# Performance work log

Hardware: AMD Instinct MI355X
Metric: run time of the kernel (lower is better)

## Reference

```python
import jax, jax.numpy as jnp
import numpy as np

EPS = 1e-6

def _rms_norm(x, w):
    # torch: x / (||x||_2 * n^{-1/2} + eps) * w
    rms = jnp.linalg.norm(x, axis=-1, keepdims=True) * (x.shape[-1] ** -0.5)
    return x / (rms + EPS) * w

def _rope_cos_sin(seq_len, head_dim):
    half = head_dim // 2
    freq = 1.0 / (10000.0 ** (jnp.arange(half, dtype=jnp.float32) / half))
    t = jnp.arange(seq_len, dtype=jnp.float32)
    freqs = t[:, None] * freq[None, :]            # [s, half]
    freqs = jnp.concatenate([freqs, freqs], -1)   # [s, d_head]
    cos = jnp.cos(freqs)[None, :, None, :]        # [1, s, 1, d_head]
    sin = jnp.sin(freqs)[None, :, None, :]
    return cos, sin

def _rotate_half(x):
    h = x.shape[-1] // 2
    return jnp.concatenate([-x[..., h:], x[..., :h]], -1)

def setup_inputs() -> dict:
    key = jax.random.key(0)
    ks = jax.random.split(key, 8)
    B, S, D, H, F = 2, 2048, 2048, 16, 128
    return {
        'query_input': jax.random.normal(ks[0], (B, S, D), jnp.float32),
        'key_input':   jax.random.normal(ks[1], (B, S, D), jnp.float32),
        'value_input': jax.random.normal(ks[2], (B, S, D), jnp.float32),
        'W_Q': jax.random.normal(ks[3], (H, D, F), jnp.float32) * (D ** -0.5),
        'W_K': jax.random.normal(ks[4], (H, D, F), jnp.float32) * (D ** -0.5),
        'W_V': jax.random.normal(ks[5], (H, D, F), jnp.float32) * (D ** -0.5),
        'W_O': jax.random.normal(ks[6], (H, F, D), jnp.float32) * (F ** -0.5),
        'b_Q': jnp.zeros((H, F), jnp.float32),
        'b_K': jnp.zeros((H, F), jnp.float32),
        'b_V': jnp.zeros((H, F), jnp.float32),
        'b_O': jnp.zeros((D,), jnp.float32),
        'q_norm_w': jnp.ones((F,), jnp.float32),
        'k_norm_w': jnp.ones((F,), jnp.float32),
    }

def reference(query_input, key_input, value_input, W_Q, W_K, W_V, W_O,
              b_Q, b_K, b_V, b_O, q_norm_w, k_norm_w):
    head_dim = W_Q.shape[-1]
    q = jnp.einsum('bpd,hdf->bphf', query_input, W_Q) + b_Q[None, None]
    k = jnp.einsum('bpd,hdf->bphf', key_input,   W_K) + b_K[None, None]
    v = jnp.einsum('bpd,hdf->bphf', value_input, W_V) + b_V[None, None]
    q = _rms_norm(q, q_norm_w)
    k = _rms_norm(k, k_norm_w)
    cos, sin = _rope_cos_sin(q.shape[1], head_dim)
    q = q * cos + _rotate_half(q) * sin
    k = k * cos + _rotate_half(k) * sin
    scores = jnp.einsum('bphf,bqhf->bhpq', q, k) / (head_dim ** 0.5)
    pattern = jax.nn.softmax(scores, axis=-1)
    attn = jnp.einsum('bhpq,bqhf->bphf', pattern, v)
    return jnp.einsum('bphf,hfm->bpm', attn, W_O) + b_O
```

## Files before the change

kernel.cpp:

```cpp
#include <hip/hip_runtime.h>
#include <stdint.h>

typedef unsigned short u16;
typedef __attribute__((ext_vector_type(8))) short  s8b;
typedef __attribute__((ext_vector_type(4))) float  f32x4;

#define S_LEN   2048
#define NHEAD   16
#define HD      128
#define DM      2048
#define NB      2
#define NPLANE  (NB*NHEAD)
#define ROWS    (NB*S_LEN)
#define PLANE_ELEMS (S_LEN*HD)
#define ATT_SCALE 0.08838834764831845f
#define LOG2E     1.4426950408889634f

__device__ __forceinline__ float bf2f(u16 u){
  union { unsigned u; float f; } x; x.u = ((unsigned)u) << 16; return x.f;
}
__device__ __forceinline__ u16 f2bf(float f){
  union { float f; unsigned u; } x; x.f = f;
  unsigned r = x.u + 0x7FFFu + ((x.u >> 16) & 1u);
  return (u16)(r >> 16);
}
__device__ __forceinline__ unsigned cvtpk(float lo, float hi){
  unsigned r;
  asm("v_cvt_pk_bf16_f32 %0, %1, %2" : "=v"(r) : "v"(lo), "v"(hi));
  return r;
}

typedef const __attribute__((address_space(1))) unsigned int* gas1;
typedef __attribute__((address_space(3))) unsigned int* las3;
__device__ __forceinline__ void gload16(const void* g, void* l){
  __builtin_amdgcn_global_load_lds((gas1)g, (las3)l, 16, 0, 0);
}

__device__ __forceinline__ f32x4 mfma16(s8b a, s8b b, f32x4 c){
  return __builtin_amdgcn_mfma_f32_16x16x32_bf16(a, b, c, 0, 0, 0);
}

__global__ __launch_bounds__(256) void cvt4(const float4* __restrict__ in,
                                            uint2* __restrict__ out, int n4){
  int i = blockIdx.x*256 + threadIdx.x;
  if (i >= n4) return;
  float4 v = in[i];
  uint2 o;
  o.x = (unsigned)f2bf(v.x) | ((unsigned)f2bf(v.y) << 16);
  o.y = (unsigned)f2bf(v.z) | ((unsigned)f2bf(v.w) << 16);
  out[i] = o;
}

__global__ __launch_bounds__(256) void transpose_cvt(const float* __restrict__ in,
                                                     u16* __restrict__ out,
                                                     int R, int C, int outStride){
  __shared__ float tile[32][33];
  int z = blockIdx.z;
  const float* inz = in + (size_t)z * R * C;
  u16* outz = out + (size_t)z * C * outStride;
  int r0 = blockIdx.x*32, c0 = blockIdx.y*32;
  int tx = threadIdx.x, ty = threadIdx.y;
  #pragma unroll
  for (int i=0;i<4;i++)
    tile[ty*4+i][tx] = inz[(size_t)(r0+ty*4+i)*C + c0 + tx];
  __syncthreads();
  #pragma unroll
  for (int i=0;i<4;i++)
    outz[(size_t)(c0+ty*4+i)*outStride + r0 + tx] = f2bf(tile[tx][ty*4+i]);
}

__global__ __launch_bounds__(256) void rope_tab(float* __restrict__ ctab,
                                                float* __restrict__ stab){
  int i = blockIdx.x*256 + threadIdx.x;
  int p = i >> 6, j = i & 63;
  double freq = pow(10000.0, -(double)j / 64.0);
  double a = (double)p * freq;
  ctab[i] = (float)cos(a);
  stab[i] = (float)sin(a);
}

__global__ __launch_bounds__(256) void gemm_bt(const u16* __restrict__ A,
                                               const u16* __restrict__ BT,
                                               const float* __restrict__ bias,
                                               void* __restrict__ out, int mode){
  const int K = 2048;
  __shared__ u16 As[2][4096];
  __shared__ u16 Bs[2][4096];
  const int t = threadIdx.x, w = t >> 6, l = t & 63;
  const int lr = l & 15, lg = l >> 4;
  int bid = blockIdx.x;
  int swz = (bid & 7)*64 + (bid >> 3);
  const int M0 = (swz >> 4) * 128, N0 = (swz & 15) * 128;
  const int wr = w >> 1, wc = w & 1;

  f32x4 acc[4][4];
  #pragma unroll
  for (int i=0;i<4;i++)
    #pragma unroll
    for (int j=0;j<4;j++) acc[i][j] = f32x4{0.f,0.f,0.f,0.f};

  auto stage = [&](int buf, int kt){
    #pragma unroll
    for (int c=0;c<2;c++){
      int mloc = c*64 + w*16 + (l>>2);
      int kloc = (l&3)*8;
      gload16(A  + (size_t)(M0+mloc)*K + kt*32 + kloc, &As[buf][c*2048 + w*512]);
      gload16(BT + (size_t)(N0+mloc)*K + kt*32 + kloc, &Bs[buf][c*2048 + w*512]);
    }
  };

  stage(0, 0);
  int cur = 0;
  const int NT = K/32;
  for (int kt=0; kt<NT; kt++){
    __syncthreads();
    if (kt+1 < NT) stage(cur^1, kt+1);
    s8b af[4], bf[4];
    #pragma unroll
    for (int i=0;i<4;i++){
      af[i] = *(const s8b*)&As[cur][(wr*64 + i*16 + lr)*32 + lg*8];
      bf[i] = *(const s8b*)&Bs[cur][(wc*64 + i*16 + lr)*32 + lg*8];
    }
    __builtin_amdgcn_s_setprio(1);
    #pragma unroll
    for (int i=0;i<4;i++)
      #pragma unroll
      for (int j=0;j<4;j++)
        acc[i][j] = mfma16(af[i], bf[j], acc[i][j]);
    __builtin_amdgcn_s_setprio(0);
    cur ^= 1;
  }

  #pragma unroll
  for (int i=0;i<4;i++){
    int growb = M0 + wr*64 + i*16 + lg*4;
    #pragma unroll
    for (int j=0;j<4;j++){
      int gcol = N0 + wc*64 + j*16 + lr;
      float bv = bias[gcol];
      #pragma unroll
      for (int r=0;r<4;r++){
        int grow = growb + r;
        float v = acc[i][j][r] + bv;
        if (mode == 2){
          ((float*)out)[(size_t)grow*2048 + gcol] = v;
        } else {
          int b = grow >> 11, p = grow & 2047;
          int h = gcol >> 7,  f = gcol & 127;
          if (mode == 0){
            ((u16*)out)[(((size_t)(b*NHEAD+h))*S_LEN + p)*HD + f] = f2bf(v);
          } else {
            size_t base = ((size_t)(b*NHEAD+h)*PLANE_ELEMS + (size_t)(p>>6)*8192) * 2;
            int p6 = p & 63;
            int q_ = ((p6&12)<<1) | (p6&3) | ((p6&16)>>2);
            int kvp = (p6 & 32) | q_;
            int byte = (f*128 + kvp*2) ^ ((f&7)<<4);
            *(u16*)((char*)out + base + byte) = f2bf(v);
          }
        }
      }
    }
  }
}

__global__ __launch_bounds__(256) void norm_rope(const u16* __restrict__ in,
                                                 u16* __restrict__ outp,
                                                 const float* __restrict__ nw,
                                                 const float* __restrict__ ctab,
                                                 const float* __restrict__ stab,
                                                 int swizzled, float oscale){
  int t = threadIdx.x, w = t>>6, l = t&63;
  size_t R = (size_t)blockIdx.x*4 + w;
  int p = (int)(R & (S_LEN-1));
  size_t base = R * HD;
  float x0 = bf2f(in[base + l]);
  float x1 = bf2f(in[base + 64 + l]);
  float ss = x0*x0 + x1*x1;
  #pragma unroll
  for (int m=1;m<64;m<<=1) ss += __shfl_xor(ss, m);
  float rms = sqrtf(ss * (1.0f/128.0f));
  float sc = oscale / (rms + 1e-6f);
  float xn0 = x0 * sc * nw[l];
  float xn1 = x1 * sc * nw[64+l];
  float c = ctab[(size_t)p*64 + l], s = stab[(size_t)p*64 + l];
  float o0 = xn0*c - xn1*s;
  float o1 = xn1*c + xn0*s;
  if (!swizzled){
    outp[base + l]      = f2bf(o0);
    outp[base + 64 + l] = f2bf(o1);
  } else {
    size_t plane = R >> 11;
    int kv = p & 63;
    size_t tb = (plane*(size_t)PLANE_ELEMS + (size_t)(p>>6)*8192) * 2;
    int b0 = (kv*256 + l*2)        ^ ((kv&7)<<4);
    int b1 = (kv*256 + (64+l)*2)   ^ ((kv&7)<<4);
    *(u16*)((char*)outp + tb + b0) = f2bf(o0);
    *(u16*)((char*)outp + tb + b1) = f2bf(o1);
  }
}

__global__ __launch_bounds__(512) void attn_fwd(const u16* __restrict__ qn,
                                                const u16* __restrict__ kn,
                                                const u16* __restrict__ vt,
                                                u16* __restrict__ attn_out){
  __shared__ u16 Klds[2][8192];
  __shared__ u16 Vlds[2][8192];
  int t = threadIdx.x, w = t>>6, l = t&63;
  int lr = l&15, lg = l>>4;

  int bid = blockIdx.x;
  int xcd = bid & 7, j = bid >> 3;
  int plane = xcd*4 + (j >> 4);
  int qb = j & 15;
  int q0 = qb*128 + w*16;

  s8b qf[4];
  #pragma unroll
  for (int fc=0; fc<4; fc++)
    qf[fc] = *(const s8b*)(qn + ((size_t)plane*S_LEN + q0 + lr)*HD + fc*32 + lg*8);

  float m = -1e30f, lsum = 0.f;
  f32x4 oacc[8];
  #pragma unroll
  for (int i=0;i<8;i++) oacc[i] = f32x4{0.f,0.f,0.f,0.f};

  const u16* kbase = kn + (size_t)plane*PLANE_ELEMS;
  const u16* vbase = vt + (size_t)plane*PLANE_ELEMS;

  auto stage = [&](int buf, int kt){
    #pragma unroll
    for (int i=0;i<2;i++){
      gload16(kbase + (size_t)kt*8192 + w*1024 + i*512 + l*8, &Klds[buf][w*1024 + i*512]);
      gload16(vbase + (size_t)kt*8192 + w*1024 + i*512 + l*8, &Vlds[buf][w*1024 + i*512]);
    }
  };

  stage(0, 0);
  int cur = 0;
  for (int kt=0; kt<32; kt++){
    __syncthreads();
    if (kt+1 < 32) stage(cur^1, kt+1);

    f32x4 sacc[4];
    #pragma unroll
    for (int c=0;c<4;c++) sacc[c] = f32x4{0.f,0.f,0.f,0.f};
    __builtin_amdgcn_s_setprio(1);
    #pragma unroll
    for (int c=0;c<4;c++){
      int kv = c*16 + lr;
      #pragma unroll
      for (int fc=0; fc<4; fc++){
        int byte = (kv*256 + (fc*32 + lg*8)*2) ^ ((kv&7)<<4);
        s8b kf = *(const s8b*)((const char*)&Klds[cur][0] + byte);
        sacc[c] = mfma16(kf, qf[fc], sacc[c]);
      }
    }
    __builtin_amdgcn_s_setprio(0);

    float mx01 = fmaxf(fmaxf(sacc[0][0], sacc[0][1]), fmaxf(sacc[0][2], sacc[0][3]));
    float mx11 = fmaxf(fmaxf(sacc[1][0], sacc[1][1]), fmaxf(sacc[1][2], sacc[1][3]));
    float mx21 = fmaxf(fmaxf(sacc[2][0], sacc[2][1]), fmaxf(sacc[2][2], sacc[2][3]));
    float mx31 = fmaxf(fmaxf(sacc[3][0], sacc[3][1]), fmaxf(sacc[3][2], sacc[3][3]));
    float mx = fmaxf(fmaxf(mx01, mx11), fmaxf(mx21, mx31));
    if (__any(mx > m + 11.5f)){
      float v = mx;
      v = fmaxf(v, __shfl_xor(v, 16));
      v = fmaxf(v, __shfl_xor(v, 32));
      v = fmaxf(m, v);
      float al = exp2f(m - v);
      m = v; lsum *= al;
      float alr[4];
      #pragma unroll
      for (int r=0;r<4;r++) alr[r] = __shfl(al, lg*4 + r);
      #pragma unroll
      for (int i=0;i<8;i++)
        #pragma unroll
        for (int r=0;r<4;r++) oacc[i][r] *= alr[r];
    }
    float pv[4][4];
    float ls0 = 0.f, ls1 = 0.f, ls2 = 0.f, ls3 = 0.f;
    #pragma unroll
    for (int c=0;c<4;c++){
      float e0 = exp2f(sacc[c][0] - m);
      float e1 = exp2f(sacc[c][1] - m);
      float e2 = exp2f(sacc[c][2] - m);
      float e3 = exp2f(sacc[c][3] - m);
      pv[c][0]=e0; pv[c][1]=e1; pv[c][2]=e2; pv[c][3]=e3;
      ls0 += e0; ls1 += e1; ls2 += e2; ls3 += e3;
    }
    lsum += (ls0 + ls1) + (ls2 + ls3);

    s8b pa[2];
    #pragma unroll
    for (int kc=0;kc<2;kc++){
      union { s8b v; unsigned u[4]; } pu;
      pu.u[0] = cvtpk(pv[2*kc][0],   pv[2*kc][1]);
      pu.u[1] = cvtpk(pv[2*kc][2],   pv[2*kc][3]);
      pu.u[2] = cvtpk(pv[2*kc+1][0], pv[2*kc+1][1]);
      pu.u[3] = cvtpk(pv[2*kc+1][2], pv[2*kc+1][3]);
      pa[kc] = pu.v;
    }

    __builtin_amdgcn_s_setprio(1);
    #pragma unroll
    for (int kc=0;kc<2;kc++){
      #pragma unroll
      for (int fc2=0; fc2<8; fc2++){
        int f = fc2*16 + lr;
        int byte = (f*128 + (kc*32 + lg*8)*2) ^ ((f&7)<<4);
        s8b vf = *(const s8b*)((const char*)&Vlds[cur][0] + byte);
        oacc[fc2] = mfma16(pa[kc], vf, oacc[fc2]);
      }
    }
    __builtin_amdgcn_s_setprio(0);
    cur ^= 1;
  }

  {
    float v = lsum;
    v += __shfl_xor(v, 16);
    v += __shfl_xor(v, 32);
    lsum = 1.0f / v;
  }
  float lir[4];
  #pragma unroll
  for (int r=0;r<4;r++) lir[r] = __shfl(lsum, lg*4 + r);
  int b = plane >> 4, h = plane & 15;
  #pragma unroll
  for (int fc2=0; fc2<8; fc2++){
    int f = fc2*16 + lr;
    #pragma unroll
    for (int r=0;r<4;r++){
      int row = q0 + lg*4 + r;
      float v = oacc[fc2][r] * lir[r];
      attn_out[(((size_t)b*S_LEN + row)*NHEAD + h)*HD + f] = f2bf(v);
    }
  }
}

extern "C" void kernel_launch(void* const* d_in, const int* in_sizes, int n_in,
                              void* d_out, int out_size, void* d_ws, size_t ws_size,
                              hipStream_t stream){
  const float* xq = (const float*)d_in[0];
  const float* xk = (const float*)d_in[1];
  const float* xv = (const float*)d_in[2];
  const float* WQ = (const float*)d_in[3];
  const float* WK = (const float*)d_in[4];
  const float* WV = (const float*)d_in[5];
  const float* WO = (const float*)d_in[6];
  const float* bQ = (const float*)d_in[7];
  const float* bK = (const float*)d_in[8];
  const float* bV = (const float*)d_in[9];
  const float* bO = (const float*)d_in[10];
  const float* qw = (const float*)d_in[11];
  const float* kw = (const float*)d_in[12];

  char* ws = (char*)d_ws;
  size_t off = 0;
  auto alloc = [&](size_t bytes)->void*{
    void* p = ws + off; off += (bytes + 255) & ~(size_t)255; return p;
  };
  const size_t ACT = (size_t)ROWS*DM*2;
  const size_t WMT = (size_t)DM*DM*2;
  u16* xqb  = (u16*)alloc(ACT);
  u16* xkb  = (u16*)alloc(ACT);
  u16* xvb  = (u16*)alloc(ACT);
  u16* WqT  = (u16*)alloc(WMT);
  u16* WkT  = (u16*)alloc(WMT);
  u16* WvT  = (u16*)alloc(WMT);
  u16* WoT  = (u16*)alloc(WMT);
  u16* qraw = (u16*)alloc(ACT);
  u16* kraw = (u16*)alloc(ACT);
  u16* knT  = (u16*)alloc(ACT);
  u16* vtS  = (u16*)alloc(ACT);
  u16* attn = (u16*)alloc(ACT);
  float* ctab = (float*)alloc((size_t)S_LEN*64*4);
  float* stab = (float*)alloc((size_t)S_LEN*64*4);
  if (off > ws_size) return;

  const int n4 = ROWS*DM/4;
  cvt4<<<dim3(n4/256), dim3(256), 0, stream>>>((const float4*)xq, (uint2*)xqb, n4);
  cvt4<<<dim3(n4/256), dim3(256), 0, stream>>>((const float4*)xk, (uint2*)xkb, n4);
  cvt4<<<dim3(n4/256), dim3(256), 0, stream>>>((const float4*)xv, (uint2*)xvb, n4);
  rope_tab<<<dim3(S_LEN*64/256), dim3(256), 0, stream>>>(ctab, stab);
  transpose_cvt<<<dim3(64,4,16), dim3(32,8), 0, stream>>>(WQ, WqT, 2048, 128, 2048);
  transpose_cvt<<<dim3(64,4,16), dim3(32,8), 0, stream>>>(WK, WkT, 2048, 128, 2048);
  transpose_cvt<<<dim3(64,4,16), dim3(32,8), 0, stream>>>(WV, WvT, 2048, 128, 2048);
  transpose_cvt<<<dim3(64,64,1), dim3(32,8), 0, stream>>>(WO, WoT, 2048, 2048, 2048);

  gemm_bt<<<dim3(512), dim3(256), 0, stream>>>(xqb, WqT, bQ, qraw, 0);
  gemm_bt<<<dim3(512), dim3(256), 0, stream>>>(xkb, WkT, bK, kraw, 0);
  gemm_bt<<<dim3(512), dim3(256), 0, stream>>>(xvb, WvT, bV, vtS, 1);

  norm_rope<<<dim3(NPLANE*S_LEN/4), dim3(256), 0, stream>>>(qraw, qraw, qw, ctab, stab, 0, ATT_SCALE*LOG2E);
  norm_rope<<<dim3(NPLANE*S_LEN/4), dim3(256), 0, stream>>>(kraw, knT, kw, ctab, stab, 1, 1.0f);

  attn_fwd<<<dim3(512), dim3(512), 0, stream>>>(qraw, knT, vtS, attn);

  gemm_bt<<<dim3(512), dim3(256), 0, stream>>>(attn, WoT, bO, d_out, 2);
}
```

Measured before the change: 397.2 us.

## Merge input conversions, use float rope table, unroll GEMM and attention loops by two

Folds the three fp32-to-bf16 input conversion launches into a single launch that picks its tensor from blockIdx.y, cutting launch overhead. The rope table now uses single-precision exp2f/cosf/sinf in place of double-precision pow/cos/sin, which is cheaper but slightly less accurate at large angles. The GEMM and attention main loops are unrolled by two with fixed double-buffer indices, removing the runtime buffer toggle and the per-iteration bound check on the first stage call.

```diff
diff --git a/kernel.cpp b/kernel.cpp
--- a/kernel.cpp
+++ b/kernel.cpp
@@ -40,15 +40,21 @@
   return __builtin_amdgcn_mfma_f32_16x16x32_bf16(a, b, c, 0, 0, 0);
 }
 
-__global__ __launch_bounds__(256) void cvt4(const float4* __restrict__ in,
-                                            uint2* __restrict__ out, int n4){
+__global__ __launch_bounds__(256) void cvt4x3(const float4* __restrict__ a,
+                                              const float4* __restrict__ b,
+                                              const float4* __restrict__ c,
+                                              uint2* __restrict__ oa,
+                                              uint2* __restrict__ ob,
+                                              uint2* __restrict__ oc, int n4){
   int i = blockIdx.x*256 + threadIdx.x;
   if (i >= n4) return;
-  float4 v = in[i];
+  const float4* src = (blockIdx.y == 0) ? a : (blockIdx.y == 1) ? b : c;
+  uint2*       dst  = (blockIdx.y == 0) ? oa : (blockIdx.y == 1) ? ob : oc;
+  float4 v = src[i];
   uint2 o;
   o.x = (unsigned)f2bf(v.x) | ((unsigned)f2bf(v.y) << 16);
   o.y = (unsigned)f2bf(v.z) | ((unsigned)f2bf(v.w) << 16);
-  out[i] = o;
+  dst[i] = o;
 }
 
 __global__ __launch_bounds__(256) void transpose_cvt(const float* __restrict__ in,
@@ -73,10 +79,10 @@
                                                 float* __restrict__ stab){
   int i = blockIdx.x*256 + threadIdx.x;
   int p = i >> 6, j = i & 63;
-  double freq = pow(10000.0, -(double)j / 64.0);
-  double a = (double)p * freq;
-  ctab[i] = (float)cos(a);
-  stab[i] = (float)sin(a);
+  float freq = exp2f(-(float)j * (13.287712379549449f/64.0f));
+  float a = (float)p * freq;
+  ctab[i] = cosf(a);
+  stab[i] = sinf(a);
 }
 
 __global__ __launch_bounds__(256) void gemm_bt(const u16* __restrict__ A,
@@ -109,27 +115,34 @@
     }
   };
 
+#define GBODY(CUR) { \
+    s8b af[4], bf[4]; \
+    _Pragma("unroll") \
+    for (int i=0;i<4;i++){ \
+      af[i] = *(const s8b*)&As[CUR][(wr*64 + i*16 + lr)*32 + lg*8]; \
+      bf[i] = *(const s8b*)&Bs[CUR][(wc*64 + i*16 + lr)*32 + lg*8]; \
+    } \
+    __builtin_amdgcn_s_setprio(1); \
+    _Pragma("unroll") \
+    for (int i=0;i<4;i++) \
+      _Pragma("unroll") \
+      for (int j=0;j<4;j++) \
+        acc[i][j] = mfma16(af[i], bf[j], acc[i][j]); \
+    __builtin_amdgcn_s_setprio(0); \
+  }
+
   stage(0, 0);
-  int cur = 0;
   const int NT = K/32;
-  for (int kt=0; kt<NT; kt++){
+  for (int kt2=0; kt2<NT/2; kt2++){
+    int kt = kt2*2;
     __syncthreads();
-    if (kt+1 < NT) stage(cur^1, kt+1);
-    s8b af[4], bf[4];
-    #pragma unroll
-    for (int i=0;i<4;i++){
-      af[i] = *(const s8b*)&As[cur][(wr*64 + i*16 + lr)*32 + lg*8];
-      bf[i] = *(const s8b*)&Bs[cur][(wc*64 + i*16 + lr)*32 + lg*8];
-    }
-    __builtin_amdgcn_s_setprio(1);
-    #pragma unroll
-    for (int i=0;i<4;i++)
-      #pragma unroll
-      for (int j=0;j<4;j++)
-        acc[i][j] = mfma16(af[i], bf[j], acc[i][j]);
-    __builtin_amdgcn_s_setprio(0);
-    cur ^= 1;
-  }
+    stage(1, kt+1);
+    GBODY(0);
+    __syncthreads();
+    if (kt+2 < NT) stage(0, kt+2);
+    GBODY(1);
+  }
+#undef GBODY
 
   #pragma unroll
   for (int i=0;i<4;i++){
@@ -235,86 +248,89 @@
     }
   };
 
+#define ATILE(CUR) { \
+    f32x4 sacc[4]; \
+    _Pragma("unroll") \
+    for (int c=0;c<4;c++) sacc[c] = f32x4{0.f,0.f,0.f,0.f}; \
+    __builtin_amdgcn_s_setprio(1); \
+    _Pragma("unroll") \
+    for (int c=0;c<4;c++){ \
+      int kv = c*16 + lr; \
+      _Pragma("unroll") \
+      for (int fc=0; fc<4; fc++){ \
+        int byte = (kv*256 + (fc*32 + lg*8)*2) ^ ((kv&7)<<4); \
+        s8b kf = *(const s8b*)((const char*)&Klds[CUR][0] + byte); \
+        sacc[c] = mfma16(kf, qf[fc], sacc[c]); \
+      } \
+    } \
+    __builtin_amdgcn_s_setprio(0); \
+    float mx01 = fmaxf(fmaxf(sacc[0][0], sacc[0][1]), fmaxf(sacc[0][2], sacc[0][3])); \
+    float mx11 = fmaxf(fmaxf(sacc[1][0], sacc[1][1]), fmaxf(sacc[1][2], sacc[1][3])); \
+    float mx21 = fmaxf(fmaxf(sacc[2][0], sacc[2][1]), fmaxf(sacc[2][2], sacc[2][3])); \
+    float mx31 = fmaxf(fmaxf(sacc[3][0], sacc[3][1]), fmaxf(sacc[3][2], sacc[3][3])); \
+    float mx = fmaxf(fmaxf(mx01, mx11), fmaxf(mx21, mx31)); \
+    if (__any(mx > m + 11.5f)){ \
+      float v = mx; \
+      v = fmaxf(v, __shfl_xor(v, 16)); \
+      v = fmaxf(v, __shfl_xor(v, 32)); \
+      v = fmaxf(m, v); \
+      float al = exp2f(m - v); \
+      m = v; lsum *= al; \
+      float alr[4]; \
+      _Pragma("unroll") \
+      for (int r=0;r<4;r++) alr[r] = __shfl(al, lg*4 + r); \
+      _Pragma("unroll") \
+      for (int i=0;i<8;i++) \
+        _Pragma("unroll") \
+        for (int r=0;r<4;r++) oacc[i][r] *= alr[r]; \
+    } \
+    float pv[4][4]; \
+    float ls0 = 0.f, ls1 = 0.f, ls2 = 0.f, ls3 = 0.f; \
+    _Pragma("unroll") \
+    for (int c=0;c<4;c++){ \
+      float e0 = exp2f(sacc[c][0] - m); \
+      float e1 = exp2f(sacc[c][1] - m); \
+      float e2 = exp2f(sacc[c][2] - m); \
+      float e3 = exp2f(sacc[c][3] - m); \
+      pv[c][0]=e0; pv[c][1]=e1; pv[c][2]=e2; pv[c][3]=e3; \
+      ls0 += e0; ls1 += e1; ls2 += e2; ls3 += e3; \
+    } \
+    lsum += (ls0 + ls1) + (ls2 + ls3); \
+    s8b pa[2]; \
+    _Pragma("unroll") \
+    for (int kc=0;kc<2;kc++){ \
+      union { s8b v; unsigned u[4]; } pu; \
+      pu.u[0] = cvtpk(pv[2*kc][0],   pv[2*kc][1]); \
+      pu.u[1] = cvtpk(pv[2*kc][2],   pv[2*kc][3]); \
+      pu.u[2] = cvtpk(pv[2*kc+1][0], pv[2*kc+1][1]); \
+      pu.u[3] = cvtpk(pv[2*kc+1][2], pv[2*kc+1][3]); \
+      pa[kc] = pu.v; \
+    } \
+    __builtin_amdgcn_s_setprio(1); \
+    _Pragma("unroll") \
+    for (int kc=0;kc<2;kc++){ \
+      _Pragma("unroll") \
+      for (int fc2=0; fc2<8; fc2++){ \
+        int f = fc2*16 + lr; \
+        int byte = (f*128 + (kc*32 + lg*8)*2) ^ ((f&7)<<4); \
+        s8b vf = *(const s8b*)((const char*)&Vlds[CUR][0] + byte); \
+        oacc[fc2] = mfma16(pa[kc], vf, oacc[fc2]); \
+      } \
+    } \
+    __builtin_amdgcn_s_setprio(0); \
+  }
+
   stage(0, 0);
-  int cur = 0;
-  for (int kt=0; kt<32; kt++){
+  for (int kt2=0; kt2<16; kt2++){
+    int kt = kt2*2;
     __syncthreads();
-    if (kt+1 < 32) stage(cur^1, kt+1);
-
-    f32x4 sacc[4];
-    #pragma unroll
-    for (int c=0;c<4;c++) sacc[c] = f32x4{0.f,0.f,0.f,0.f};
-    __builtin_amdgcn_s_setprio(1);
-    #pragma unroll
-    for (int c=0;c<4;c++){
-      int kv = c*16 + lr;
-      #pragma unroll
-      for (int fc=0; fc<4; fc++){
-        int byte = (kv*256 + (fc*32 + lg*8)*2) ^ ((kv&7)<<4);
-        s8b kf = *(const s8b*)((const char*)&Klds[cur][0] + byte);
-        sacc[c] = mfma16(kf, qf[fc], sacc[c]);
-      }
-    }
-    __builtin_amdgcn_s_setprio(0);
-
-    float mx01 = fmaxf(fmaxf(sacc[0][0], sacc[0][1]), fmaxf(sacc[0][2], sacc[0][3]));
-    float mx11 = fmaxf(fmaxf(sacc[1][0], sacc[1][1]), fmaxf(sacc[1][2], sacc[1][3]));
-    float mx21 = fmaxf(fmaxf(sacc[2][0], sacc[2][1]), fmaxf(sacc[2][2], sacc[2][3]));
-    float mx31 = fmaxf(fmaxf(sacc[3][0], sacc[3][1]), fmaxf(sacc[3][2], sacc[3][3]));
-    float mx = fmaxf(fmaxf(mx01, mx11), fmaxf(mx21, mx31));
-    if (__any(mx > m + 11.5f)){
-      float v = mx;
-      v = fmaxf(v, __shfl_xor(v, 16));
-      v = fmaxf(v, __shfl_xor(v, 32));
-      v = fmaxf(m, v);
-      float al = exp2f(m - v);
-      m = v; lsum *= al;
-      float alr[4];
-      #pragma unroll
-      for (int r=0;r<4;r++) alr[r] = __shfl(al, lg*4 + r);
-      #pragma unroll
-      for (int i=0;i<8;i++)
-        #pragma unroll
-        for (int r=0;r<4;r++) oacc[i][r] *= alr[r];
-    }
-    float pv[4][4];
-    float ls0 = 0.f, ls1 = 0.f, ls2 = 0.f, ls3 = 0.f;
-    #pragma unroll
-    for (int c=0;c<4;c++){
-      float e0 = exp2f(sacc[c][0] - m);
-      float e1 = exp2f(sacc[c][1] - m);
-      float e2 = exp2f(sacc[c][2] - m);
-      float e3 = exp2f(sacc[c][3] - m);
-      pv[c][0]=e0; pv[c][1]=e1; pv[c][2]=e2; pv[c][3]=e3;
-      ls0 += e0; ls1 += e1; ls2 += e2; ls3 += e3;
-    }
-    lsum += (ls0 + ls1) + (ls2 + ls3);
-
-    s8b pa[2];
-    #pragma unroll
-    for (int kc=0;kc<2;kc++){
-      union { s8b v; unsigned u[4]; } pu;
-      pu.u[0] = cvtpk(pv[2*kc][0],   pv[2*kc][1]);
-      pu.u[1] = cvtpk(pv[2*kc][2],   pv[2*kc][3]);
-      pu.u[2] = cvtpk(pv[2*kc+1][0], pv[2*kc+1][1]);
-      pu.u[3] = cvtpk(pv[2*kc+1][2], pv[2*kc+1][3]);
-      pa[kc] = pu.v;
-    }
-
-    __builtin_amdgcn_s_setprio(1);
-    #pragma unroll
-    for (int kc=0;kc<2;kc++){
-      #pragma unroll
-      for (int fc2=0; fc2<8; fc2++){
-        int f = fc2*16 + lr;
-        int byte = (f*128 + (kc*32 + lg*8)*2) ^ ((f&7)<<4);
-        s8b vf = *(const s8b*)((const char*)&Vlds[cur][0] + byte);
-        oacc[fc2] = mfma16(pa[kc], vf, oacc[fc2]);
-      }
-    }
-    __builtin_amdgcn_s_setprio(0);
-    cur ^= 1;
-  }
+    stage(1, kt+1);
+    ATILE(0);
+    __syncthreads();
+    if (kt+2 < 32) stage(0, kt+2);
+    ATILE(1);
+  }
+#undef ATILE
 
   {
     float v = lsum;
@@ -379,9 +395,9 @@
   if (off > ws_size) return;
 
   const int n4 = ROWS*DM/4;
-  cvt4<<<dim3(n4/256), dim3(256), 0, stream>>>((const float4*)xq, (uint2*)xqb, n4);
-  cvt4<<<dim3(n4/256), dim3(256), 0, stream>>>((const float4*)xk, (uint2*)xkb, n4);
-  cvt4<<<dim3(n4/256), dim3(256), 0, stream>>>((const float4*)xv, (uint2*)xvb, n4);
+  cvt4x3<<<dim3(n4/256, 3), dim3(256), 0, stream>>>((const float4*)xq, (const float4*)xk,
+                                                    (const float4*)xv, (uint2*)xqb,
+                                                    (uint2*)xkb, (uint2*)xvb, n4);
   rope_tab<<<dim3(S_LEN*64/256), dim3(256), 0, stream>>>(ctab, stab);
   transpose_cvt<<<dim3(64,4,16), dim3(32,8), 0, stream>>>(WQ, WqT, 2048, 128, 2048);
   transpose_cvt<<<dim3(64,4,16), dim3(32,8), 0, stream>>>(WK, WkT, 2048, 128, 2048);
```

New measurement: 416.8 us. 4.9% more time.

## Process two query tiles per attention wave, merge input converts, float rope table

Applied to the files above, without the earlier changes.

The attention kernel now runs 4 waves instead of 8, and each wave handles 32 query rows as two 16-row tiles. Each K and V fragment read from LDS then feeds two MFMAs, which halves LDS traffic per unit of math. The cost is more accumulator registers, which may lower occupancy; launch bounds are set to 2 blocks per CU. Separately, the three activation convert launches are merged into one 2D-grid launch, and the rope table uses float exp2f/cosf/sinf instead of double precision, which risks small accuracy differences at large angles.

```diff
diff --git a/kernel.cpp b/kernel.cpp
--- a/kernel.cpp
+++ b/kernel.cpp
@@ -40,15 +40,21 @@
   return __builtin_amdgcn_mfma_f32_16x16x32_bf16(a, b, c, 0, 0, 0);
 }
 
-__global__ __launch_bounds__(256) void cvt4(const float4* __restrict__ in,
-                                            uint2* __restrict__ out, int n4){
+__global__ __launch_bounds__(256) void cvt4x3(const float4* __restrict__ a,
+                                              const float4* __restrict__ b,
+                                              const float4* __restrict__ c,
+                                              uint2* __restrict__ oa,
+                                              uint2* __restrict__ ob,
+                                              uint2* __restrict__ oc, int n4){
   int i = blockIdx.x*256 + threadIdx.x;
   if (i >= n4) return;
-  float4 v = in[i];
+  const float4* src = (blockIdx.y == 0) ? a : (blockIdx.y == 1) ? b : c;
+  uint2*       dst  = (blockIdx.y == 0) ? oa : (blockIdx.y == 1) ? ob : oc;
+  float4 v = src[i];
   uint2 o;
   o.x = (unsigned)f2bf(v.x) | ((unsigned)f2bf(v.y) << 16);
   o.y = (unsigned)f2bf(v.z) | ((unsigned)f2bf(v.w) << 16);
-  out[i] = o;
+  dst[i] = o;
 }
 
 __global__ __launch_bounds__(256) void transpose_cvt(const float* __restrict__ in,
@@ -73,10 +79,10 @@
                                                 float* __restrict__ stab){
   int i = blockIdx.x*256 + threadIdx.x;
   int p = i >> 6, j = i & 63;
-  double freq = pow(10000.0, -(double)j / 64.0);
-  double a = (double)p * freq;
-  ctab[i] = (float)cos(a);
-  stab[i] = (float)sin(a);
+  float freq = exp2f(-(float)j * (13.287712379549449f/64.0f));
+  float a = (float)p * freq;
+  ctab[i] = cosf(a);
+  stab[i] = sinf(a);
 }
 
 __global__ __launch_bounds__(256) void gemm_bt(const u16* __restrict__ A,
@@ -199,10 +205,10 @@
   }
 }
 
-__global__ __launch_bounds__(512) void attn_fwd(const u16* __restrict__ qn,
-                                                const u16* __restrict__ kn,
-                                                const u16* __restrict__ vt,
-                                                u16* __restrict__ attn_out){
+__global__ __launch_bounds__(256,2) void attn_fwd(const u16* __restrict__ qn,
+                                                  const u16* __restrict__ kn,
+                                                  const u16* __restrict__ vt,
+                                                  u16* __restrict__ attn_out){
   __shared__ u16 Klds[2][8192];
   __shared__ u16 Vlds[2][8192];
   int t = threadIdx.x, w = t>>6, l = t&63;
@@ -212,26 +218,32 @@
   int xcd = bid & 7, j = bid >> 3;
   int plane = xcd*4 + (j >> 4);
   int qb = j & 15;
-  int q0 = qb*128 + w*16;
-
-  s8b qf[4];
-  #pragma unroll
-  for (int fc=0; fc<4; fc++)
-    qf[fc] = *(const s8b*)(qn + ((size_t)plane*S_LEN + q0 + lr)*HD + fc*32 + lg*8);
-
-  float m = -1e30f, lsum = 0.f;
-  f32x4 oacc[8];
-  #pragma unroll
-  for (int i=0;i<8;i++) oacc[i] = f32x4{0.f,0.f,0.f,0.f};
+  int q0 = qb*128 + w*32;
+
+  s8b qf[2][4];
+  #pragma unroll
+  for (int qi=0; qi<2; qi++)
+    #pragma unroll
+    for (int fc=0; fc<4; fc++)
+      qf[qi][fc] = *(const s8b*)(qn + ((size_t)plane*S_LEN + q0 + qi*16 + lr)*HD + fc*32 + lg*8);
+
+  float m[2], lsum[2];
+  #pragma unroll
+  for (int qi=0;qi<2;qi++){ m[qi] = -1e30f; lsum[qi] = 0.f; }
+  f32x4 oacc[2][8];
+  #pragma unroll
+  for (int qi=0;qi<2;qi++)
+    #pragma unroll
+    for (int i=0;i<8;i++) oacc[qi][i] = f32x4{0.f,0.f,0.f,0.f};
 
   const u16* kbase = kn + (size_t)plane*PLANE_ELEMS;
   const u16* vbase = vt + (size_t)plane*PLANE_ELEMS;
 
   auto stage = [&](int buf, int kt){
     #pragma unroll
-    for (int i=0;i<2;i++){
-      gload16(kbase + (size_t)kt*8192 + w*1024 + i*512 + l*8, &Klds[buf][w*1024 + i*512]);
-      gload16(vbase + (size_t)kt*8192 + w*1024 + i*512 + l*8, &Vlds[buf][w*1024 + i*512]);
+    for (int i=0;i<4;i++){
+      gload16(kbase + (size_t)kt*8192 + w*2048 + i*512 + l*8, &Klds[buf][w*2048 + i*512]);
+      gload16(vbase + (size_t)kt*8192 + w*2048 + i*512 + l*8, &Vlds[buf][w*2048 + i*512]);
     }
   };
 
@@ -241,9 +253,11 @@
     __syncthreads();
     if (kt+1 < 32) stage(cur^1, kt+1);
 
-    f32x4 sacc[4];
-    #pragma unroll
-    for (int c=0;c<4;c++) sacc[c] = f32x4{0.f,0.f,0.f,0.f};
+    f32x4 sacc[4][2];
+    #pragma unroll
+    for (int c=0;c<4;c++)
+      #pragma unroll
+      for (int qi=0;qi<2;qi++) sacc[c][qi] = f32x4{0.f,0.f,0.f,0.f};
     __builtin_amdgcn_s_setprio(1);
     #pragma unroll
     for (int c=0;c<4;c++){
@@ -252,54 +266,68 @@
       for (int fc=0; fc<4; fc++){
         int byte = (kv*256 + (fc*32 + lg*8)*2) ^ ((kv&7)<<4);
         s8b kf = *(const s8b*)((const char*)&Klds[cur][0] + byte);
-        sacc[c] = mfma16(kf, qf[fc], sacc[c]);
+        sacc[c][0] = mfma16(kf, qf[0][fc], sacc[c][0]);
+        sacc[c][1] = mfma16(kf, qf[1][fc], sacc[c][1]);
       }
     }
     __builtin_amdgcn_s_setprio(0);
 
-    float mx01 = fmaxf(fmaxf(sacc[0][0], sacc[0][1]), fmaxf(sacc[0][2], sacc[0][3]));
-    float mx11 = fmaxf(fmaxf(sacc[1][0], sacc[1][1]), fmaxf(sacc[1][2], sacc[1][3]));
-    float mx21 = fmaxf(fmaxf(sacc[2][0], sacc[2][1]), fmaxf(sacc[2][2], sacc[2][3]));
-    float mx31 = fmaxf(fmaxf(sacc[3][0], sacc[3][1]), fmaxf(sacc[3][2], sacc[3][3]));
-    float mx = fmaxf(fmaxf(mx01, mx11), fmaxf(mx21, mx31));
-    if (__any(mx > m + 11.5f)){
-      float v = mx;
-      v = fmaxf(v, __shfl_xor(v, 16));
-      v = fmaxf(v, __shfl_xor(v, 32));
-      v = fmaxf(m, v);
-      float al = exp2f(m - v);
-      m = v; lsum *= al;
-      float alr[4];
-      #pragma unroll
-      for (int r=0;r<4;r++) alr[r] = __shfl(al, lg*4 + r);
-      #pragma unroll
-      for (int i=0;i<8;i++)
+    float mx[2];
+    #pragma unroll
+    for (int qi=0;qi<2;qi++){
+      float a0 = fmaxf(fmaxf(sacc[0][qi][0], sacc[0][qi][1]), fmaxf(sacc[0][qi][2], sacc[0][qi][3]));
+      float a1 = fmaxf(fmaxf(sacc[1][qi][0], sacc[1][qi][1]), fmaxf(sacc[1][qi][2], sacc[1][qi][3]));
+      float a2 = fmaxf(fmaxf(sacc[2][qi][0], sacc[2][qi][1]), fmaxf(sacc[2][qi][2], sacc[2][qi][3]));
+      float a3 = fmaxf(fmaxf(sacc[3][qi][0], sacc[3][qi][1]), fmaxf(sacc[3][qi][2], sacc[3][qi][3]));
+      mx[qi] = fmaxf(fmaxf(a0, a1), fmaxf(a2, a3));
+    }
+    bool need = (mx[0] > m[0] + 11.5f) || (mx[1] > m[1] + 11.5f);
+    if (__any(need)){
+      #pragma unroll
+      for (int qi=0;qi<2;qi++){
+        float v = mx[qi];
+        v = fmaxf(v, __shfl_xor(v, 16));
+        v = fmaxf(v, __shfl_xor(v, 32));
+        v = fmaxf(m[qi], v);
+        float al = exp2f(m[qi] - v);
+        m[qi] = v; lsum[qi] *= al;
+        float alr[4];
         #pragma unroll
-        for (int r=0;r<4;r++) oacc[i][r] *= alr[r];
-    }
-    float pv[4][4];
-    float ls0 = 0.f, ls1 = 0.f, ls2 = 0.f, ls3 = 0.f;
-    #pragma unroll
-    for (int c=0;c<4;c++){
-      float e0 = exp2f(sacc[c][0] - m);
-      float e1 = exp2f(sacc[c][1] - m);
-      float e2 = exp2f(sacc[c][2] - m);
-      float e3 = exp2f(sacc[c][3] - m);
-      pv[c][0]=e0; pv[c][1]=e1; pv[c][2]=e2; pv[c][3]=e3;
-      ls0 += e0; ls1 += e1; ls2 += e2; ls3 += e3;
-    }
-    lsum += (ls0 + ls1) + (ls2 + ls3);
-
-    s8b pa[2];
-    #pragma unroll
-    for (int kc=0;kc<2;kc++){
-      union { s8b v; unsigned u[4]; } pu;
-      pu.u[0] = cvtpk(pv[2*kc][0],   pv[2*kc][1]);
-      pu.u[1] = cvtpk(pv[2*kc][2],   pv[2*kc][3]);
-      pu.u[2] = cvtpk(pv[2*kc+1][0], pv[2*kc+1][1]);
-      pu.u[3] = cvtpk(pv[2*kc+1][2], pv[2*kc+1][3]);
-      pa[kc] = pu.v;
-    }
+        for (int r=0;r<4;r++) alr[r] = __shfl(al, lg*4 + r);
+        #pragma unroll
+        for (int i=0;i<8;i++)
+          #pragma unroll
+          for (int r=0;r<4;r++) oacc[qi][i][r] *= alr[r];
+      }
+    }
+    float pv[2][4][4];
+    #pragma unroll
+    for (int qi=0;qi<2;qi++){
+      float ls0=0.f, ls1=0.f, ls2=0.f, ls3=0.f;
+      #pragma unroll
+      for (int c=0;c<4;c++){
+        float e0 = exp2f(sacc[c][qi][0] - m[qi]);
+        float e1 = exp2f(sacc[c][qi][1] - m[qi]);
+        float e2 = exp2f(sacc[c][qi][2] - m[qi]);
+        float e3 = exp2f(sacc[c][qi][3] - m[qi]);
+        pv[qi][c][0]=e0; pv[qi][c][1]=e1; pv[qi][c][2]=e2; pv[qi][c][3]=e3;
+        ls0 += e0; ls1 += e1; ls2 += e2; ls3 += e3;
+      }
+      lsum[qi] += (ls0 + ls1) + (ls2 + ls3);
+    }
+
+    s8b pa[2][2];
+    #pragma unroll
+    for (int qi=0;qi<2;qi++)
+      #pragma unroll
+      for (int kc=0;kc<2;kc++){
+        union { s8b v; unsigned u[4]; } pu;
+        pu.u[0] = cvtpk(pv[qi][2*kc][0],   pv[qi][2*kc][1]);
+        pu.u[1] = cvtpk(pv[qi][2*kc][2],   pv[qi][2*kc][3]);
+        pu.u[2] = cvtpk(pv[qi][2*kc+1][0], pv[qi][2*kc+1][1]);
+        pu.u[3] = cvtpk(pv[qi][2*kc+1][2], pv[qi][2*kc+1][3]);
+        pa[qi][kc] = pu.v;
+      }
 
     __builtin_amdgcn_s_setprio(1);
     #pragma unroll
@@ -309,31 +337,33 @@
         int f = fc2*16 + lr;
         int byte = (f*128 + (kc*32 + lg*8)*2) ^ ((f&7)<<4);
         s8b vf = *(const s8b*)((const char*)&Vlds[cur][0] + byte);
-        oacc[fc2] = mfma16(pa[kc], vf, oacc[fc2]);
+        oacc[0][fc2] = mfma16(pa[0][kc], vf, oacc[0][fc2]);
+        oacc[1][fc2] = mfma16(pa[1][kc], vf, oacc[1][fc2]);
       }
     }
     __builtin_amdgcn_s_setprio(0);
     cur ^= 1;
   }
 
-  {
-    float v = lsum;
+  int b = plane >> 4, h = plane & 15;
+  #pragma unroll
+  for (int qi=0;qi<2;qi++){
+    float v = lsum[qi];
     v += __shfl_xor(v, 16);
     v += __shfl_xor(v, 32);
-    lsum = 1.0f / v;
-  }
-  float lir[4];
-  #pragma unroll
-  for (int r=0;r<4;r++) lir[r] = __shfl(lsum, lg*4 + r);
-  int b = plane >> 4, h = plane & 15;
-  #pragma unroll
-  for (int fc2=0; fc2<8; fc2++){
-    int f = fc2*16 + lr;
-    #pragma unroll
-    for (int r=0;r<4;r++){
-      int row = q0 + lg*4 + r;
-      float v = oacc[fc2][r] * lir[r];
-      attn_out[(((size_t)b*S_LEN + row)*NHEAD + h)*HD + f] = f2bf(v);
+    v = 1.0f / v;
+    float lir[4];
+    #pragma unroll
+    for (int r=0;r<4;r++) lir[r] = __shfl(v, lg*4 + r);
+    #pragma unroll
+    for (int fc2=0; fc2<8; fc2++){
+      int f = fc2*16 + lr;
+      #pragma unroll
+      for (int r=0;r<4;r++){
+        int row = q0 + qi*16 + lg*4 + r;
+        float o = oacc[qi][fc2][r] * lir[r];
+        attn_out[(((size_t)b*S_LEN + row)*NHEAD + h)*HD + f] = f2bf(o);
+      }
     }
   }
 }
@@ -379,9 +409,9 @@
   if (off > ws_size) return;
 
   const int n4 = ROWS*DM/4;
-  cvt4<<<dim3(n4/256), dim3(256), 0, stream>>>((const float4*)xq, (uint2*)xqb, n4);
-  cvt4<<<dim3(n4/256), dim3(256), 0, stream>>>((const float4*)xk, (uint2*)xkb, n4);
-  cvt4<<<dim3(n4/256), dim3(256), 0, stream>>>((const float4*)xv, (uint2*)xvb, n4);
+  cvt4x3<<<dim3(n4/256, 3), dim3(256), 0, stream>>>((const float4*)xq, (const float4*)xk,
+                                                    (const float4*)xv, (uint2*)xqb,
+                                                    (uint2*)xkb, (uint2*)xvb, n4);
   rope_tab<<<dim3(S_LEN*64/256), dim3(256), 0, stream>>>(ctab, stab);
   transpose_cvt<<<dim3(64,4,16), dim3(32,8), 0, stream>>>(WQ, WqT, 2048, 128, 2048);
   transpose_cvt<<<dim3(64,4,16), dim3(32,8), 0, stream>>>(WK, WkT, 2048, 128, 2048);
@@ -395,7 +425,7 @@
   norm_rope<<<dim3(NPLANE*S_LEN/4), dim3(256), 0, stream>>>(qraw, qraw, qw, ctab, stab, 0, ATT_SCALE*LOG2E);
   norm_rope<<<dim3(NPLANE*S_LEN/4), dim3(256), 0, stream>>>(kraw, knT, kw, ctab, stab, 1, 1.0f);
 
-  attn_fwd<<<dim3(512), dim3(512), 0, stream>>>(qraw, knT, vtS, attn);
+  attn_fwd<<<dim3(512), dim3(256), 0, stream>>>(qraw, knT, vtS, attn);
 
   gemm_bt<<<dim3(512), dim3(256), 0, stream>>>(attn, WoT, bO, d_out, 2);
 }
```

After: 375.7 us. 5.4% less time.
